# Kernel tuning notes

Hardware: AMD Instinct MI355X
Metric: run time of the kernel (lower is better)

Reference implementation:

```python
import jax, jax.numpy as jnp
import numpy as np

K = 3  # adaptive kernel size
M = 4  # channel reduction


def setup_inputs() -> dict:
    key = jax.random.key(0)
    ks = jax.random.split(key, 10)
    N, C, H, W = 32, 512, 48, 48
    Cm = C // M            # 128
    P = 512                # planes
    sc = 0.05
    x   = jax.random.normal(ks[0], (N, C, H, W), jnp.float32)
    Wc  = jax.random.normal(ks[1], (Cm, C), jnp.float32) * sc   # conv 1x1 (C->Cm)
    bc  = jax.random.normal(ks[2], (Cm,), jnp.float32) * sc
    Wkk = jax.random.normal(ks[3], (K * K,), jnp.float32) * sc  # conv_kernel (1->k*k, 1x1)
    bkk = jax.random.normal(ks[4], (K * K,), jnp.float32) * sc
    Wck = jax.random.normal(ks[5], (Cm, 2), jnp.float32) * sc   # conv_k (2->Cm, 1x1)
    bck = jax.random.normal(ks[6], (Cm,), jnp.float32) * sc
    b_ad = jax.random.normal(ks[7], (Cm,), jnp.float32) * sc    # conv_adap_kernel bias (learned)
    Wf  = jax.random.normal(ks[8], (P, Cm), jnp.float32) * sc   # fuse 1x1 (Cm->planes)
    bf  = jax.random.normal(ks[9], (P,), jnp.float32) * sc
    return {"x": x, "Wc": Wc, "bc": bc, "Wkk": Wkk, "bkk": bkk,
            "Wck": Wck, "bck": bck, "b_ad": b_ad, "Wf": Wf, "bf": bf}


def reference(x, Wc, bc, Wkk, bkk, Wck, bck, b_ad, Wf, bf):
    N, C, H, W = x.shape
    Cm = Wc.shape[0]
    k = K
    pad = (k - 1) // 2

    # f = relu(conv1x1(x)) -> [N, Cm, H, W]
    f = jax.nn.relu(jnp.einsum('oc,nchw->nohw', Wc, x) + bc[None, :, None, None])

    # global branch: adaptive avg pool to 1 -> shared conv1x1 -> relu -> [N, Cm]
    gk1 = jax.nn.relu(jnp.mean(x, axis=(2, 3)) @ Wc.T + bc)
    # conv_kernel (1->k*k 1x1 over permuted layout): per-channel affine into k*k values
    g_kern = (gk1[:, :, None] * Wkk[None, None, :] + bkk[None, None, :]).reshape(N, Cm, k, k)

    # spatial branch: adaptive max pool to k x k (H,W divisible by k) -> shared conv1x1 -> relu
    xm = x.reshape(N, C, k, H // k, k, W // k).max(axis=(3, 5))  # [N, C, k, k]
    sk = jax.nn.relu(jnp.einsum('oc,nckl->nokl', Wc, xm) + bc[None, :, None, None])

    # kernel generation: conv_k (2->Cm 1x1) over [g_kern, sk], then the permute makes
    # weight[o, c, :, :] = relu(sum_j Wck[o, j] * gs[c, j, :, :] + bck[o])
    gs = jnp.stack([g_kern, sk], axis=2)  # [N, Cm, 2, k, k]
    dynW = jax.nn.relu(jnp.einsum('oj,ncjkl->nockl', Wck, gs)
                       + bck[None, :, None, None, None])  # [N, Cm_out, Cm_in, k, k]

    # per-sample dynamic conv2d, vectorized over batch
    def conv_one(fn, wn):
        return jax.lax.conv_general_dilated(
            fn[None], wn, window_strides=(1, 1),
            padding=[(pad, pad), (pad, pad)])[0]

    y = jax.vmap(conv_one)(f, dynW) + b_ad[None, :, None, None]  # [N, Cm, H, W]

    # fuse 1x1 -> planes
    out = jnp.einsum('oc,nchw->nohw', Wf, y) + bf[None, :, None, None]
    return out
```

## Files before the change

### kernel.cpp

```cpp
#include <hip/hip_runtime.h>

#define N_   32
#define C_   512
#define CM_  128
#define H_   48
#define W_   48
#define HW_  (H_*W_)
#define P_   512

typedef unsigned short ushort_t;
typedef short s8v  __attribute__((ext_vector_type(8)));
typedef float f4v  __attribute__((ext_vector_type(4)));

__device__ __forceinline__ ushort_t f2bf(float x) {
    unsigned int u = __float_as_uint(x);
    u += 0x7fffu + ((u >> 16) & 1u);
    return (ushort_t)(u >> 16);
}

__global__ __launch_bounds__(256) void pool_kernel(const float* __restrict__ x,
                                                   float* __restrict__ meanx,
                                                   float* __restrict__ xm,
                                                   const float* __restrict__ Wc,
                                                   const float* __restrict__ Wf,
                                                   ushort_t* __restrict__ Wc_bf,
                                                   ushort_t* __restrict__ Wf_bf) {
    if (blockIdx.x >= N_ * C_) {
        int idx = (blockIdx.x - N_ * C_) * 256 + threadIdx.x;
        float4 v;
        ushort_t* dst;
        if (idx < 16384) {
            v = ((const float4*)Wc)[idx];
            dst = Wc_bf + (size_t)idx * 4;
        } else {
            int k = idx - 16384;
            v = ((const float4*)Wf)[k];
            dst = Wf_bf + (size_t)k * 4;
        }
        uint2 pk;
        pk.x = (unsigned)f2bf(v.x) | ((unsigned)f2bf(v.y) << 16);
        pk.y = (unsigned)f2bf(v.z) | ((unsigned)f2bf(v.w) << 16);
        *(uint2*)dst = pk;
        return;
    }
    int plane = blockIdx.x;
    const float* base = x + (size_t)plane * HW_;
    int t = threadIdx.x;
    int r = t >> 4, cc = t & 15;
    float sum = 0.f;
    float mx[9];
#pragma unroll
    for (int b = 0; b < 9; ++b) {
        int h = (b / 3) * 16 + r;
        int w = (b % 3) * 16 + cc;
        float v = base[h * W_ + w];
        mx[b] = v;
        sum += v;
    }
#pragma unroll
    for (int off = 32; off > 0; off >>= 1) {
        sum += __shfl_down(sum, off);
#pragma unroll
        for (int b = 0; b < 9; ++b) mx[b] = fmaxf(mx[b], __shfl_down(mx[b], off));
    }
    __shared__ float s[4][10];
    int wave = t >> 6, lane = t & 63;
    if (lane == 0) {
#pragma unroll
        for (int b = 0; b < 9; ++b) s[wave][b] = mx[b];
        s[wave][9] = sum;
    }
    __syncthreads();
    if (t < 9) {
        float v = fmaxf(fmaxf(s[0][t], s[1][t]), fmaxf(s[2][t], s[3][t]));
        xm[(size_t)plane * 9 + t] = v;
    } else if (t == 9) {
        float v = s[0][9] + s[1][9] + s[2][9] + s[3][9];
        meanx[plane] = v * (1.0f / (float)HW_);
    }
}

__global__ __launch_bounds__(512) void branch_kernel(const float* __restrict__ meanx,
                                                     const float* __restrict__ xm,
                                                     const float* __restrict__ Wc,
                                                     const float* __restrict__ bc,
                                                     const float* __restrict__ Wkk,
                                                     const float* __restrict__ bkk,
                                                     float* __restrict__ gs) {
    int n = blockIdx.x;
    __shared__ float sin_[C_ * 10];
    __shared__ float Ws[4][128][17];
    int t = threadIdx.x;
    for (int i = t; i < C_ * 10; i += 512) {
        int c = i / 10, j = i % 10;
        sin_[i] = (j < 9) ? xm[((size_t)n * C_ + c) * 9 + j] : meanx[n * C_ + c];
    }
    int o = t & 127, p = t >> 7;
    float acc[10];
#pragma unroll
    for (int j = 0; j < 10; ++j) acc[j] = 0.f;

    for (int s = 0; s < 8; ++s) {
        __syncthreads();
#pragma unroll
        for (int k = 0; k < 4; ++k) {
            int f = t + k * 512;
            int chunk = f >> 9, oo = (f >> 2) & 127, col4 = f & 3;
            float4 v = *(const float4*)(Wc + (size_t)oo * C_ + chunk * 128 + s * 16 + col4 * 4);
            *(float4*)&Ws[chunk][oo][col4 * 4] = v;
        }
        __syncthreads();
        int cbase = p * 128 + s * 16;
#pragma unroll
        for (int cc = 0; cc < 16; ++cc) {
            float wv = Ws[p][o][cc];
            const float* in = &sin_[(cbase + cc) * 10];
#pragma unroll
            for (int j = 0; j < 10; ++j) acc[j] += wv * in[j];
        }
    }
    __syncthreads();
    float* red = (float*)Ws;
#pragma unroll
    for (int j = 0; j < 10; ++j) red[t * 10 + j] = acc[j];
    __syncthreads();
    if (t < 128) {
        float a[10];
#pragma unroll
        for (int j = 0; j < 10; ++j)
            a[j] = red[t * 10 + j] + red[1280 + t * 10 + j]
                 + red[2560 + t * 10 + j] + red[3840 + t * 10 + j];
        float bco = bc[t];
        float gk1 = fmaxf(a[9] + bco, 0.f);
        size_t gbase = (size_t)n * 18 * CM_;
#pragma unroll
        for (int b = 0; b < 9; ++b) {
            gs[gbase + b * CM_ + t]       = gk1 * Wkk[b] + bkk[b];
            gs[gbase + (9 + b) * CM_ + t] = fmaxf(a[b] + bco, 0.f);
        }
    }
}

__global__ __launch_bounds__(256) void dynw_kernel(const float* __restrict__ gs,
                                                   const float* __restrict__ Wck,
                                                   const float* __restrict__ bck,
                                                   ushort_t* __restrict__ dynW_t) {
    int idx = blockIdx.x * 256 + threadIdx.x;
    int c8 = idx & 15;
    int o  = (idx >> 4) & 127;
    int v  = idx >> 11;
    int r  = v % 9;
    int n  = v / 9;
    const float* gp = gs + ((size_t)n * 18 + r) * CM_ + c8 * 8;
    float w0 = Wck[o * 2], w1 = Wck[o * 2 + 1], bk = bck[o];
    ushort_t u[8];
#pragma unroll
    for (int i = 0; i < 8; ++i) {
        float g = gp[i];
        float s = gp[9 * CM_ + i];
        u[i] = f2bf(fmaxf(w0 * g + w1 * s + bk, 0.f));
    }
    uint4 pk;
    pk.x = (unsigned)u[0] | ((unsigned)u[1] << 16);
    pk.y = (unsigned)u[2] | ((unsigned)u[3] << 16);
    pk.z = (unsigned)u[4] | ((unsigned)u[5] << 16);
    pk.w = (unsigned)u[6] | ((unsigned)u[7] << 16);
    *(uint4*)(dynW_t + (size_t)idx * 8) = pk;
}

__global__ __launch_bounds__(256) void fconv_mfma(const float* __restrict__ x,
                                                  const ushort_t* __restrict__ Wc_bf,
                                                  const float* __restrict__ bc,
                                                  ushort_t* __restrict__ f_t) {
    int n = blockIdx.y;
    int hw0 = blockIdx.x * 64;
    __shared__ ushort_t Bs[64 * 40];
    int t = threadIdx.x;
    int wave = t >> 6, lane = t & 63;
    int j = lane & 15, q = lane >> 4;
    int o_w = wave * 32;
    int sk  = t >> 4;
    int shw = (t & 15) * 4;

    const s8v* A = (const s8v*)Wc_bf;
    f4v acc[2][4];
#pragma unroll
    for (int mt = 0; mt < 2; ++mt)
#pragma unroll
        for (int nt = 0; nt < 4; ++nt) acc[mt][nt] = (f4v){0.f, 0.f, 0.f, 0.f};

    for (int c0 = 0; c0 < C_; c0 += 32) {
        const float* xr = x + ((size_t)n * C_ + c0 + 2 * sk) * HW_ + hw0 + shw;
        float4 v0 = *(const float4*)xr;
        float4 v1 = *(const float4*)(xr + HW_);
        __syncthreads();
        unsigned* Bw = (unsigned*)Bs;
        {
            unsigned w0 = (unsigned)f2bf(v0.x) | ((unsigned)f2bf(v1.x) << 16);
            unsigned w1 = (unsigned)f2bf(v0.y) | ((unsigned)f2bf(v1.y) << 16);
            unsigned w2 = (unsigned)f2bf(v0.z) | ((unsigned)f2bf(v1.z) << 16);
            unsigned w3 = (unsigned)f2bf(v0.w) | ((unsigned)f2bf(v1.w) << 16);
            Bw[(shw + 0) * 20 + sk] = w0;
            Bw[(shw + 1) * 20 + sk] = w1;
            Bw[(shw + 2) * 20 + sk] = w2;
            Bw[(shw + 3) * 20 + sk] = w3;
        }
        __syncthreads();
        s8v a0 = A[(size_t)(o_w + j) * 64 + (c0 >> 3) + q];
        s8v a1 = A[(size_t)(o_w + 16 + j) * 64 + (c0 >> 3) + q];
        s8v b[4];
#pragma unroll
        for (int nt = 0; nt < 4; ++nt)
            b[nt] = *(const s8v*)&Bs[(nt * 16 + j) * 40 + q * 8];
#pragma unroll
        for (int nt = 0; nt < 4; ++nt) {
            acc[0][nt] = __builtin_amdgcn_mfma_f32_16x16x32_bf16(a0, b[nt], acc[0][nt], 0, 0, 0);
            acc[1][nt] = __builtin_amdgcn_mfma_f32_16x16x32_bf16(a1, b[nt], acc[1][nt], 0, 0, 0);
        }
    }
#pragma unroll
    for (int mt = 0; mt < 2; ++mt) {
        int ob = o_w + mt * 16 + q * 4;
        float b4[4];
#pragma unroll
        for (int reg = 0; reg < 4; ++reg) b4[reg] = bc[ob + reg];
#pragma unroll
        for (int nt = 0; nt < 4; ++nt) {
            int hw = hw0 + nt * 16 + j;
            ushort_t u[4];
#pragma unroll
            for (int reg = 0; reg < 4; ++reg)
                u[reg] = f2bf(fmaxf(acc[mt][nt][reg] + b4[reg], 0.f));
            uint2 pk;
            pk.x = (unsigned)u[0] | ((unsigned)u[1] << 16);
            pk.y = (unsigned)u[2] | ((unsigned)u[3] << 16);
            *(uint2*)(f_t + ((size_t)n * HW_ + hw) * CM_ + ob) = pk;
        }
    }
}

__global__ __launch_bounds__(256, 3) void dynconv_mfma(const ushort_t* __restrict__ f_t,
                                                       const ushort_t* __restrict__ dynW_t,
                                                       const float* __restrict__ b_ad,
                                                       ushort_t* __restrict__ y_bf) {
    __shared__ ushort_t Bs[4 * 50 * 128];
    int bid = blockIdx.x;
    int vid = (bid & 7) * 96 + (bid >> 3);
    int n   = vid / 24;
    int h0  = (vid % 24) * 2;
    int t = threadIdx.x;
    int wave = t >> 6, lane = t & 63;
    int j = lane & 15, q = lane >> 4;

    if (t < 128) {
        int ri = t >> 5, wi = ((t >> 4) & 1) * 49, ci = t & 15;
        int off = ((ri * 50 + wi) * 256 + ci * 16) ^ ((wi & 7) << 4);
        uint4 z; z.x = 0u; z.y = 0u; z.z = 0u; z.w = 0u;
        *(uint4*)((char*)Bs + off) = z;
    }
#pragma unroll
    for (int ri = 0; ri < 4; ++ri) {
        int h = h0 - 1 + ri;
        bool hok = (unsigned)h < (unsigned)H_;
        const uint4* src = (const uint4*)(f_t + ((size_t)n * HW_ + h * W_) * CM_);
#pragma unroll
        for (int s = 0; s < 3; ++s) {
            int c2 = s * 256 + t;
            int wi = (c2 >> 4) + 1, ci = c2 & 15;
            uint4 v; v.x = 0u; v.y = 0u; v.z = 0u; v.w = 0u;
            if (hok) v = src[c2];
            int off = ((ri * 50 + wi) * 256 + ci * 16) ^ ((wi & 7) << 4);
            *(uint4*)((char*)Bs + off) = v;
        }
    }
    __syncthreads();

    int ow = wave * 32;
    const s8v* A = (const s8v*)dynW_t;
    size_t abase = ((size_t)n * 9 * 128 + ow + j) * 16 + q;

    f4v acc[2][6];
#pragma unroll
    for (int mt = 0; mt < 2; ++mt)
#pragma unroll
        for (int nt = 0; nt < 6; ++nt) acc[mt][nt] = (f4v){0.f, 0.f, 0.f, 0.f};

    for (int cc = 0; cc < 4; ++cc) {
        s8v a[9][2];
#pragma unroll
        for (int r = 0; r < 9; ++r) {
            a[r][0] = A[abase + (size_t)r * 2048 + cc * 4];
            a[r][1] = A[abase + (size_t)r * 2048 + 256 + cc * 4];
        }
#pragma unroll
        for (int ri = 0; ri < 4; ++ri) {
#pragma unroll
            for (int dwi = 0; dwi < 3; ++dwi) {
                int xr = ((j + dwi) & 7) << 4;
#pragma unroll
                for (int wg = 0; wg < 3; ++wg) {
                    int wi = wg * 16 + j + dwi;
                    int off = ((ri * 50 + wi) * 256 + cc * 64 + q * 16) ^ xr;
                    s8v b = *(const s8v*)((const char*)Bs + off);
                    if (ri < 3) {
                        int r = ri * 3 + dwi;
                        acc[0][wg] = __builtin_amdgcn_mfma_f32_16x16x32_bf16(a[r][0], b, acc[0][wg], 0, 0, 0);
                        acc[1][wg] = __builtin_amdgcn_mfma_f32_16x16x32_bf16(a[r][1], b, acc[1][wg], 0, 0, 0);
                    }
                    if (ri > 0) {
                        int r = (ri - 1) * 3 + dwi;
                        acc[0][3 + wg] = __builtin_amdgcn_mfma_f32_16x16x32_bf16(a[r][0], b, acc[0][3 + wg], 0, 0, 0);
                        acc[1][3 + wg] = __builtin_amdgcn_mfma_f32_16x16x32_bf16(a[r][1], b, acc[1][3 + wg], 0, 0, 0);
                    }
                }
            }
        }
    }

#pragma unroll
    for (int mt = 0; mt < 2; ++mt) {
        int ob = ow + mt * 16 + q * 4;
        float ba[4];
#pragma unroll
        for (int reg = 0; reg < 4; ++reg) ba[reg] = b_ad[ob + reg];
#pragma unroll
        for (int rl = 0; rl < 2; ++rl) {
            int h = h0 + rl;
#pragma unroll
            for (int wg = 0; wg < 3; ++wg) {
                int nt = rl * 3 + wg;
                int hw = h * W_ + wg * 16 + j;
                ushort_t u[4];
#pragma unroll
                for (int reg = 0; reg < 4; ++reg)
                    u[reg] = f2bf(acc[mt][nt][reg] + ba[reg]);
                uint2 pk;
                pk.x = (unsigned)u[0] | ((unsigned)u[1] << 16);
                pk.y = (unsigned)u[2] | ((unsigned)u[3] << 16);
                *(uint2*)(y_bf + ((size_t)n * HW_ + hw) * CM_ + ob) = pk;
            }
        }
    }
}

__global__ __launch_bounds__(128) void fuse_mfma(const ushort_t* __restrict__ y_bf,
                                                 const ushort_t* __restrict__ Wf_bf,
                                                 const float* __restrict__ bf,
                                                 float* __restrict__ out) {
    int n  = blockIdx.z;
    int p0 = blockIdx.y * 64;
    int h0 = blockIdx.x * 4;
    int t = threadIdx.x;
    int wave = t >> 6, lane = t & 63;
    int j = lane & 15, q = lane >> 4;
    int rbase = h0 + wave * 2;

    const s8v* A = (const s8v*)Wf_bf;
    const s8v* B = (const s8v*)y_bf;

    f4v acc[4][6];
#pragma unroll
    for (int mt = 0; mt < 4; ++mt)
#pragma unroll
        for (int nt = 0; nt < 6; ++nt) acc[mt][nt] = (f4v){0.f, 0.f, 0.f, 0.f};

#pragma unroll
    for (int cc = 0; cc < 4; ++cc) {
        s8v a[4];
#pragma unroll
        for (int mt = 0; mt < 4; ++mt)
            a[mt] = A[(size_t)(p0 + mt * 16 + j) * 16 + cc * 4 + q];
        s8v b[6];
#pragma unroll
        for (int rl = 0; rl < 2; ++rl) {
            int h = rbase + rl;
#pragma unroll
            for (int wg = 0; wg < 3; ++wg) {
                int hw = h * W_ + wg * 16 + j;
                b[rl * 3 + wg] = B[((size_t)n * HW_ + hw) * 16 + cc * 4 + q];
            }
        }
#pragma unroll
        for (int mt = 0; mt < 4; ++mt)
#pragma unroll
            for (int nt = 0; nt < 6; ++nt)
                acc[mt][nt] = __builtin_amdgcn_mfma_f32_16x16x32_bf16(
                    a[mt], b[nt], acc[mt][nt], 0, 0, 0);
    }
#pragma unroll
    for (int mt = 0; mt < 4; ++mt) {
        int pb = p0 + mt * 16 + q * 4;
        float b4[4];
#pragma unroll
        for (int reg = 0; reg < 4; ++reg) b4[reg] = bf[pb + reg];
#pragma unroll
        for (int rl = 0; rl < 2; ++rl) {
            int h = rbase + rl;
#pragma unroll
            for (int wg = 0; wg < 3; ++wg) {
                int nt = rl * 3 + wg;
                int hw = h * W_ + wg * 16 + j;
#pragma unroll
                for (int reg = 0; reg < 4; ++reg)
                    out[((size_t)n * P_ + pb + reg) * HW_ + hw] = acc[mt][nt][reg] + b4[reg];
            }
        }
    }
}

extern "C" void kernel_launch(void* const* d_in, const int* in_sizes, int n_in,
                              void* d_out, int out_size, void* d_ws, size_t ws_size,
                              hipStream_t stream) {
    const float* x    = (const float*)d_in[0];
    const float* Wc   = (const float*)d_in[1];
    const float* bc   = (const float*)d_in[2];
    const float* Wkk  = (const float*)d_in[3];
    const float* bkk  = (const float*)d_in[4];
    const float* Wck  = (const float*)d_in[5];
    const float* bck  = (const float*)d_in[6];
    const float* b_ad = (const float*)d_in[7];
    const float* Wf   = (const float*)d_in[8];
    const float* bf   = (const float*)d_in[9];
    float* out = (float*)d_out;

    char* ws = (char*)d_ws;
    float*    meanx  = (float*)(ws);
    float*    xm     = (float*)(ws + 65536);
    float*    gs     = (float*)(ws + 655360);
    ushort_t* dynW_t = (ushort_t*)(ws + 950272);
    ushort_t* f_t    = (ushort_t*)(ws + 10387456);
    ushort_t* y_bf   = (ushort_t*)(ws + 29261824);
    ushort_t* Wc_bf  = (ushort_t*)(ws + 48136192);
    ushort_t* Wf_bf  = (ushort_t*)(ws + 48267264);

    hipLaunchKernelGGL(pool_kernel,    dim3(N_ * C_ + 192), dim3(256), 0, stream,
                       x, meanx, xm, Wc, Wf, Wc_bf, Wf_bf);
    hipLaunchKernelGGL(branch_kernel,  dim3(N_),      dim3(512), 0, stream, meanx, xm, Wc, bc, Wkk, bkk, gs);
    hipLaunchKernelGGL(dynw_kernel,    dim3(2304),    dim3(256), 0, stream, gs, Wck, bck, dynW_t);
    hipLaunchKernelGGL(fconv_mfma,     dim3(36, 32),  dim3(256), 0, stream, x, Wc_bf, bc, f_t);
    hipLaunchKernelGGL(dynconv_mfma,   dim3(768),     dim3(256), 0, stream, f_t, dynW_t, b_ad, y_bf);
    hipLaunchKernelGGL(fuse_mfma,      dim3(12, 8, 32), dim3(128), 0, stream, y_bf, Wf_bf, bf, out);
}
```

Before: 390.7 us.

## Fuse dynW generation into branch kernel, pipeline fconv loads, stage y in LDS for fuse

Three separate changes. The dynamic-weight generation is folded into the branch kernel, with gs kept in shared memory, which removes one launch and a global round trip; the cost is that only 32 blocks now produce all of dynW. The 1x1 conv GEMM gets double-buffered LDS and register prefetch of the next x/weight tiles, so one barrier per iteration is dropped and loads overlap the MFMAs. The fuse GEMM now stages two rows of y into XOR-swizzled LDS shared by four waves covering 256 output planes, and uses a remapped block order, cutting redundant global reads of y.

```diff
diff --git a/kernel.cpp b/kernel.cpp
--- a/kernel.cpp
+++ b/kernel.cpp
@@ -86,7 +86,9 @@
                                                      const float* __restrict__ bc,
                                                      const float* __restrict__ Wkk,
                                                      const float* __restrict__ bkk,
-                                                     float* __restrict__ gs) {
+                                                     const float* __restrict__ Wck,
+                                                     const float* __restrict__ bck,
+                                                     ushort_t* __restrict__ dynW_t) {
     int n = blockIdx.x;
     __shared__ float sin_[C_ * 10];
     __shared__ float Ws[4][128][17];
@@ -124,6 +126,7 @@
 #pragma unroll
     for (int j = 0; j < 10; ++j) red[t * 10 + j] = acc[j];
     __syncthreads();
+    float* sgs = sin_;
     if (t < 128) {
         float a[10];
 #pragma unroll
@@ -132,40 +135,31 @@
                  + red[2560 + t * 10 + j] + red[3840 + t * 10 + j];
         float bco = bc[t];
         float gk1 = fmaxf(a[9] + bco, 0.f);
-        size_t gbase = (size_t)n * 18 * CM_;
 #pragma unroll
         for (int b = 0; b < 9; ++b) {
-            gs[gbase + b * CM_ + t]       = gk1 * Wkk[b] + bkk[b];
-            gs[gbase + (9 + b) * CM_ + t] = fmaxf(a[b] + bco, 0.f);
-        }
-    }
-}
-
-__global__ __launch_bounds__(256) void dynw_kernel(const float* __restrict__ gs,
-                                                   const float* __restrict__ Wck,
-                                                   const float* __restrict__ bck,
-                                                   ushort_t* __restrict__ dynW_t) {
-    int idx = blockIdx.x * 256 + threadIdx.x;
-    int c8 = idx & 15;
-    int o  = (idx >> 4) & 127;
-    int v  = idx >> 11;
-    int r  = v % 9;
-    int n  = v / 9;
-    const float* gp = gs + ((size_t)n * 18 + r) * CM_ + c8 * 8;
-    float w0 = Wck[o * 2], w1 = Wck[o * 2 + 1], bk = bck[o];
-    ushort_t u[8];
-#pragma unroll
-    for (int i = 0; i < 8; ++i) {
-        float g = gp[i];
-        float s = gp[9 * CM_ + i];
-        u[i] = f2bf(fmaxf(w0 * g + w1 * s + bk, 0.f));
-    }
-    uint4 pk;
-    pk.x = (unsigned)u[0] | ((unsigned)u[1] << 16);
-    pk.y = (unsigned)u[2] | ((unsigned)u[3] << 16);
-    pk.z = (unsigned)u[4] | ((unsigned)u[5] << 16);
-    pk.w = (unsigned)u[6] | ((unsigned)u[7] << 16);
-    *(uint4*)(dynW_t + (size_t)idx * 8) = pk;
+            sgs[b * 128 + t]       = gk1 * Wkk[b] + bkk[b];
+            sgs[(9 + b) * 128 + t] = fmaxf(a[b] + bco, 0.f);
+        }
+    }
+    __syncthreads();
+    ushort_t* dwn = dynW_t + (size_t)n * 147456;
+    for (int s = 0; s < 36; ++s) {
+        int q2 = s * 512 + t;
+        int c8 = q2 & 15, oo = (q2 >> 4) & 127, r = q2 >> 11;
+        float w0 = Wck[oo * 2], w1 = Wck[oo * 2 + 1], bk = bck[oo];
+        const float* gp = sgs + r * 128 + c8 * 8;
+        const float* sp = sgs + (9 + r) * 128 + c8 * 8;
+        ushort_t u[8];
+#pragma unroll
+        for (int i = 0; i < 8; ++i)
+            u[i] = f2bf(fmaxf(w0 * gp[i] + w1 * sp[i] + bk, 0.f));
+        uint4 pk;
+        pk.x = (unsigned)u[0] | ((unsigned)u[1] << 16);
+        pk.y = (unsigned)u[2] | ((unsigned)u[3] << 16);
+        pk.z = (unsigned)u[4] | ((unsigned)u[5] << 16);
+        pk.w = (unsigned)u[6] | ((unsigned)u[7] << 16);
+        *(uint4*)(dwn + (size_t)q2 * 8) = pk;
+    }
 }
 
 __global__ __launch_bounds__(256) void fconv_mfma(const float* __restrict__ x,
@@ -174,7 +168,7 @@
                                                   ushort_t* __restrict__ f_t) {
     int n = blockIdx.y;
     int hw0 = blockIdx.x * 64;
-    __shared__ ushort_t Bs[64 * 40];
+    __shared__ ushort_t Bs[2][64 * 40];
     int t = threadIdx.x;
     int wave = t >> 6, lane = t & 63;
     int j = lane & 15, q = lane >> 4;
@@ -183,40 +177,47 @@
     int shw = (t & 15) * 4;
 
     const s8v* A = (const s8v*)Wc_bf;
+    const float* xbase = x + ((size_t)n * C_ + 2 * sk) * HW_ + hw0 + shw;
+    size_t arow0 = (size_t)(o_w + j) * 64 + q;
+    size_t arow1 = (size_t)(o_w + 16 + j) * 64 + q;
+
     f4v acc[2][4];
 #pragma unroll
     for (int mt = 0; mt < 2; ++mt)
 #pragma unroll
         for (int nt = 0; nt < 4; ++nt) acc[mt][nt] = (f4v){0.f, 0.f, 0.f, 0.f};
 
-    for (int c0 = 0; c0 < C_; c0 += 32) {
-        const float* xr = x + ((size_t)n * C_ + c0 + 2 * sk) * HW_ + hw0 + shw;
-        float4 v0 = *(const float4*)xr;
-        float4 v1 = *(const float4*)(xr + HW_);
+    float4 v0 = *(const float4*)xbase;
+    float4 v1 = *(const float4*)(xbase + HW_);
+    s8v a0 = A[arow0];
+    s8v a1 = A[arow1];
+
+#pragma unroll 2
+    for (int k = 0; k < 16; ++k) {
+        unsigned* Bw = (unsigned*)Bs[k & 1];
+        Bw[(shw + 0) * 20 + sk] = (unsigned)f2bf(v0.x) | ((unsigned)f2bf(v1.x) << 16);
+        Bw[(shw + 1) * 20 + sk] = (unsigned)f2bf(v0.y) | ((unsigned)f2bf(v1.y) << 16);
+        Bw[(shw + 2) * 20 + sk] = (unsigned)f2bf(v0.z) | ((unsigned)f2bf(v1.z) << 16);
+        Bw[(shw + 3) * 20 + sk] = (unsigned)f2bf(v0.w) | ((unsigned)f2bf(v1.w) << 16);
         __syncthreads();
-        unsigned* Bw = (unsigned*)Bs;
-        {
-            unsigned w0 = (unsigned)f2bf(v0.x) | ((unsigned)f2bf(v1.x) << 16);
-            unsigned w1 = (unsigned)f2bf(v0.y) | ((unsigned)f2bf(v1.y) << 16);
-            unsigned w2 = (unsigned)f2bf(v0.z) | ((unsigned)f2bf(v1.z) << 16);
-            unsigned w3 = (unsigned)f2bf(v0.w) | ((unsigned)f2bf(v1.w) << 16);
-            Bw[(shw + 0) * 20 + sk] = w0;
-            Bw[(shw + 1) * 20 + sk] = w1;
-            Bw[(shw + 2) * 20 + sk] = w2;
-            Bw[(shw + 3) * 20 + sk] = w3;
-        }
-        __syncthreads();
-        s8v a0 = A[(size_t)(o_w + j) * 64 + (c0 >> 3) + q];
-        s8v a1 = A[(size_t)(o_w + 16 + j) * 64 + (c0 >> 3) + q];
+        float4 v0n, v1n; s8v a0n, a1n;
+        if (k < 15) {
+            const float* xr = xbase + (size_t)(k + 1) * 32 * HW_;
+            v0n = *(const float4*)xr;
+            v1n = *(const float4*)(xr + HW_);
+            a0n = A[arow0 + (k + 1) * 4];
+            a1n = A[arow1 + (k + 1) * 4];
+        }
         s8v b[4];
 #pragma unroll
         for (int nt = 0; nt < 4; ++nt)
-            b[nt] = *(const s8v*)&Bs[(nt * 16 + j) * 40 + q * 8];
+            b[nt] = *(const s8v*)&Bs[k & 1][(nt * 16 + j) * 40 + q * 8];
 #pragma unroll
         for (int nt = 0; nt < 4; ++nt) {
             acc[0][nt] = __builtin_amdgcn_mfma_f32_16x16x32_bf16(a0, b[nt], acc[0][nt], 0, 0, 0);
             acc[1][nt] = __builtin_amdgcn_mfma_f32_16x16x32_bf16(a1, b[nt], acc[1][nt], 0, 0, 0);
         }
+        if (k < 15) { v0 = v0n; v1 = v1n; a0 = a0n; a1 = a1n; }
     }
 #pragma unroll
     for (int mt = 0; mt < 2; ++mt) {
@@ -343,43 +344,55 @@
     }
 }
 
-__global__ __launch_bounds__(128) void fuse_mfma(const ushort_t* __restrict__ y_bf,
-                                                 const ushort_t* __restrict__ Wf_bf,
-                                                 const float* __restrict__ bf,
-                                                 float* __restrict__ out) {
-    int n  = blockIdx.z;
-    int p0 = blockIdx.y * 64;
-    int h0 = blockIdx.x * 4;
+__global__ __launch_bounds__(256, 3) void fuse_mfma(const ushort_t* __restrict__ y_bf,
+                                                    const ushort_t* __restrict__ Wf_bf,
+                                                    const float* __restrict__ bf,
+                                                    float* __restrict__ out) {
+    __shared__ ushort_t ys[2 * 48 * 128];
+    int bid = blockIdx.x;
+    int vid = (bid & 7) * 192 + (bid >> 3);
+    int n   = vid / 48;
+    int rem = vid % 48;
+    int h0  = (rem >> 1) * 2;
+    int P0  = (rem & 1) * 256;
     int t = threadIdx.x;
     int wave = t >> 6, lane = t & 63;
     int j = lane & 15, q = lane >> 4;
-    int rbase = h0 + wave * 2;
+    int p0w = P0 + wave * 64;
+
+    const uint4* src = (const uint4*)(y_bf + ((size_t)n * HW_ + h0 * W_) * CM_);
+#pragma unroll
+    for (int s = 0; s < 6; ++s) {
+        int c2 = s * 256 + t;
+        int wp = c2 >> 4, ci = c2 & 15;
+        int off = (wp * 256 + ci * 16) ^ ((wp & 7) << 4);
+        *(uint4*)((char*)ys + off) = src[c2];
+    }
+    __syncthreads();
 
     const s8v* A = (const s8v*)Wf_bf;
-    const s8v* B = (const s8v*)y_bf;
-
     f4v acc[4][6];
 #pragma unroll
     for (int mt = 0; mt < 4; ++mt)
 #pragma unroll
         for (int nt = 0; nt < 6; ++nt) acc[mt][nt] = (f4v){0.f, 0.f, 0.f, 0.f};
 
+    int xr = (j & 7) << 4;
 #pragma unroll
     for (int cc = 0; cc < 4; ++cc) {
         s8v a[4];
 #pragma unroll
         for (int mt = 0; mt < 4; ++mt)
-            a[mt] = A[(size_t)(p0 + mt * 16 + j) * 16 + cc * 4 + q];
+            a[mt] = A[(size_t)(p0w + mt * 16 + j) * 16 + cc * 4 + q];
         s8v b[6];
 #pragma unroll
-        for (int rl = 0; rl < 2; ++rl) {
-            int h = rbase + rl;
+        for (int rl = 0; rl < 2; ++rl)
 #pragma unroll
             for (int wg = 0; wg < 3; ++wg) {
-                int hw = h * W_ + wg * 16 + j;
-                b[rl * 3 + wg] = B[((size_t)n * HW_ + hw) * 16 + cc * 4 + q];
+                int wp = rl * 48 + wg * 16 + j;
+                int off = (wp * 256 + cc * 64 + q * 16) ^ xr;
+                b[rl * 3 + wg] = *(const s8v*)((const char*)ys + off);
             }
-        }
 #pragma unroll
         for (int mt = 0; mt < 4; ++mt)
 #pragma unroll
@@ -389,13 +402,13 @@
     }
 #pragma unroll
     for (int mt = 0; mt < 4; ++mt) {
-        int pb = p0 + mt * 16 + q * 4;
+        int pb = p0w + mt * 16 + q * 4;
         float b4[4];
 #pragma unroll
         for (int reg = 0; reg < 4; ++reg) b4[reg] = bf[pb + reg];
 #pragma unroll
         for (int rl = 0; rl < 2; ++rl) {
-            int h = rbase + rl;
+            int h = h0 + rl;
 #pragma unroll
             for (int wg = 0; wg < 3; ++wg) {
                 int nt = rl * 3 + wg;
@@ -426,7 +439,6 @@
     char* ws = (char*)d_ws;
     float*    meanx  = (float*)(ws);
     float*    xm     = (float*)(ws + 65536);
-    float*    gs     = (float*)(ws + 655360);
     ushort_t* dynW_t = (ushort_t*)(ws + 950272);
     ushort_t* f_t    = (ushort_t*)(ws + 10387456);
     ushort_t* y_bf   = (ushort_t*)(ws + 29261824);
@@ -435,9 +447,9 @@
 
     hipLaunchKernelGGL(pool_kernel,    dim3(N_ * C_ + 192), dim3(256), 0, stream,
                        x, meanx, xm, Wc, Wf, Wc_bf, Wf_bf);
-    hipLaunchKernelGGL(branch_kernel,  dim3(N_),      dim3(512), 0, stream, meanx, xm, Wc, bc, Wkk, bkk, gs);
-    hipLaunchKernelGGL(dynw_kernel,    dim3(2304),    dim3(256), 0, stream, gs, Wck, bck, dynW_t);
+    hipLaunchKernelGGL(branch_kernel,  dim3(N_),      dim3(512), 0, stream,
+                       meanx, xm, Wc, bc, Wkk, bkk, Wck, bck, dynW_t);
     hipLaunchKernelGGL(fconv_mfma,     dim3(36, 32),  dim3(256), 0, stream, x, Wc_bf, bc, f_t);
     hipLaunchKernelGGL(dynconv_mfma,   dim3(768),     dim3(256), 0, stream, f_t, dynW_t, b_ad, y_bf);
-    hipLaunchKernelGGL(fuse_mfma,      dim3(12, 8, 32), dim3(128), 0, stream, y_bf, Wf_bf, bf, out);
-}
+    hipLaunchKernelGGL(fuse_mfma,      dim3(1536),    dim3(256), 0, stream, y_bf, Wf_bf, bf, out);
+}
```

New measurement: 419.3 us. +7.3%, slower.
